# Optimization experiments

Measured on AMD Instinct MI355X. Metric: run time of the kernel, lower is better.

The kernel has to match this reference:

```python
import jax, jax.numpy as jnp
import numpy as np

N = 8192
IN_F = 512
OUT_F = 128
NUM_CLASSES = 10
ALPHA = 0.2  # LeakyReLU negative slope
NEG_INF = -9e15


def setup_inputs() -> dict:
    key = jax.random.key(0)
    k_h, k_d, k_W, k_a, k_cw, k_cb = jax.random.split(key, 6)
    h = jax.random.normal(k_h, (N, IN_F), dtype=jnp.float32)
    dist = jax.random.randint(k_d, (N, N), 0, 2, dtype=jnp.int32)
    # xavier_uniform with gain=1.414
    gain = 1.414
    lim_W = gain * np.sqrt(6.0 / (IN_F + OUT_F))
    W = jax.random.uniform(k_W, (IN_F, OUT_F), minval=-lim_W, maxval=lim_W, dtype=jnp.float32)
    lim_a = gain * np.sqrt(6.0 / (2 * OUT_F + 1))
    a = jax.random.uniform(k_a, (2 * OUT_F, 1), minval=-lim_a, maxval=lim_a, dtype=jnp.float32)
    # nn.Linear(out_features, num_classes): weight [C, out], bias [C]
    lim_c = np.sqrt(1.0 / OUT_F)
    Wc = jax.random.uniform(k_cw, (NUM_CLASSES, OUT_F), minval=-lim_c, maxval=lim_c, dtype=jnp.float32)
    bc = jax.random.uniform(k_cb, (NUM_CLASSES,), minval=-lim_c, maxval=lim_c, dtype=jnp.float32)
    return {"h": h, "dist": dist, "W": W, "a": a, "Wc": Wc, "bc": bc}


def reference(h, dist, W, a, Wc, bc):
    Wh = h @ W                              # [N, out]
    Wh1 = Wh @ a[:OUT_F]                    # [N, 1]
    Wh2 = Wh @ a[OUT_F:]                    # [N, 1]
    e = jax.nn.leaky_relu(Wh1 + Wh2.T, negative_slope=ALPHA)  # [N, N]
    att = jnp.where(dist > 0, e, NEG_INF)
    att = jax.nn.softmax(att, axis=1)       # [N, N]
    h_update = jax.nn.elu(att @ Wh)         # [N, out] (dropout inactive at inference)
    y_pred = h_update @ Wc.T + bc           # [N, num_classes]
    return y_pred
```

## Files before the change

### kernel.cpp

```cpp
#include <hip/hip_runtime.h>
#include <stdint.h>

#define N 8192
#define IN_F 512
#define OUT_F 128
#define NCLS 10
#define ALPHA 0.2f

typedef float f32x4 __attribute__((ext_vector_type(4)));
typedef int   i32x4 __attribute__((ext_vector_type(4)));
typedef short s16x4 __attribute__((ext_vector_type(4)));
typedef short s16x8 __attribute__((ext_vector_type(8)));

__device__ __forceinline__ short f2bf(float x) {
    unsigned u = __builtin_bit_cast(unsigned, x);
    u = (u + 0x7FFFu + ((u >> 16) & 1u)) >> 16;
    return (short)u;
}
__device__ __forceinline__ float bf2f(short s) {
    unsigned u = ((unsigned)(unsigned short)s) << 16;
    return __builtin_bit_cast(float, u);
}

__global__ __launch_bounds__(256, 8)
void mask_kernel(const int* __restrict__ dist, unsigned* __restrict__ mask) {
    size_t w = (size_t)blockIdx.x * 256 + threadIdx.x;
    const int* p = dist + w * 32;
    unsigned b = 0;
    #pragma unroll
    for (int u = 0; u < 8; ++u) {
        i32x4 v = *(const i32x4*)(p + u * 4);
        #pragma unroll
        for (int e = 0; e < 4; ++e) b |= (v[e] > 0 ? 1u : 0u) << (u * 4 + e);
    }
    mask[w] = b;
}

__global__ void split_w_kernel(const float* __restrict__ W,
                               short* __restrict__ WThi, short* __restrict__ WTlo) {
    int idx = blockIdx.x * 256 + threadIdx.x;
    int k = idx >> 7, col = idx & 127;
    float x = W[idx];
    short hi = f2bf(x);
    short lo = f2bf(x - bf2f(hi));
    size_t a = (size_t)(k >> 5) * (128 * 32) + (size_t)col * 32 + (k & 31);
    WThi[a] = hi;
    WTlo[a] = lo;
}

#define WH_ROWS 16
#define WH_STR 520

__global__ __launch_bounds__(256, 2)
void wh_kernel(const float* __restrict__ h, const short* __restrict__ WThi,
               const short* __restrict__ WTlo, const float* __restrict__ a,
               short* __restrict__ WhT, float* __restrict__ Wh1,
               float* __restrict__ Wh2) {
    __shared__ __align__(16) short Ahi[WH_ROWS][WH_STR];
    __shared__ __align__(16) short Alo[WH_ROWS][WH_STR];
    __shared__ __align__(16) float whs[WH_ROWS][OUT_F + 4];

    const int t = threadIdx.x;
    const int r0 = blockIdx.x * WH_ROWS;

    {
        int row = t >> 4, c4 = t & 15;
        const float* hrow = h + (size_t)(r0 + row) * IN_F;
        #pragma unroll
        for (int jj = 0; jj < 4; ++jj) {
            int k0 = c4 * 8 + jj * 128;
            f32x4 x0 = *(const f32x4*)(hrow + k0);
            f32x4 x1 = *(const f32x4*)(hrow + k0 + 4);
            s16x8 hi, lo;
            #pragma unroll
            for (int e = 0; e < 4; ++e) {
                short h0 = f2bf(x0[e]); hi[e] = h0; lo[e] = f2bf(x0[e] - bf2f(h0));
                short h1 = f2bf(x1[e]); hi[4 + e] = h1; lo[4 + e] = f2bf(x1[e] - bf2f(h1));
            }
            *(s16x8*)&Ahi[row][k0] = hi;
            *(s16x8*)&Alo[row][k0] = lo;
        }
    }
    __syncthreads();

    const int lane = t & 63, w = t >> 6;
    const int q = lane >> 4, ln16 = lane & 15;
    f32x4 acc[2] = {};
    #pragma unroll
    for (int kc = 0; kc < IN_F / 32; ++kc) {
        s16x8 ahi = *(const s16x8*)&Ahi[ln16][kc * 32 + q * 8];
        s16x8 alo = *(const s16x8*)&Alo[ln16][kc * 32 + q * 8];
        #pragma unroll
        for (int nt = 0; nt < 2; ++nt) {
            int col = w * 32 + nt * 16 + ln16;
            size_t boff = (size_t)kc * 4096 + (size_t)col * 32 + q * 8;
            s16x8 bhi = *(const s16x8*)(WThi + boff);
            s16x8 blo = *(const s16x8*)(WTlo + boff);
            acc[nt] = __builtin_amdgcn_mfma_f32_16x16x32_bf16(ahi, bhi, acc[nt], 0, 0, 0);
            acc[nt] = __builtin_amdgcn_mfma_f32_16x16x32_bf16(ahi, blo, acc[nt], 0, 0, 0);
            acc[nt] = __builtin_amdgcn_mfma_f32_16x16x32_bf16(alo, bhi, acc[nt], 0, 0, 0);
        }
    }
    #pragma unroll
    for (int nt = 0; nt < 2; ++nt)
        #pragma unroll
        for (int reg = 0; reg < 4; ++reg)
            whs[q * 4 + reg][w * 32 + nt * 16 + ln16] = acc[nt][reg];
    __syncthreads();

    if (t < 128) {
        int r = t >> 3, s = t & 7;
        float s1 = 0.f, s2 = 0.f;
        #pragma unroll
        for (int cc = 0; cc < 16; ++cc) {
            int c = s * 16 + cc;
            float v = whs[r][c];
            s1 = fmaf(v, a[c], s1);
            s2 = fmaf(v, a[OUT_F + c], s2);
        }
        s1 += __shfl_xor(s1, 1); s1 += __shfl_xor(s1, 2); s1 += __shfl_xor(s1, 4);
        s2 += __shfl_xor(s2, 1); s2 += __shfl_xor(s2, 2); s2 += __shfl_xor(s2, 4);
        if (s == 0) { Wh1[r0 + r] = s1; Wh2[r0 + r] = s2; }
    }

    {
        int c = t >> 1, h8 = t & 1;
        s16x8 pack;
        #pragma unroll
        for (int rr = 0; rr < 8; ++rr) pack[rr] = f2bf(whs[h8 * 8 + rr][c]);
        size_t addr = (size_t)(r0 >> 5) * 4096 + (size_t)c * 32 + (r0 & 16) + h8 * 8;
        *(s16x8*)(WhT + addr) = pack;
    }
}

#define BM 32
#define BK 256
#define ASTR (BK + 8)

__global__ __launch_bounds__(256, 4)
void attn_kernel(const unsigned* __restrict__ mask, const short* __restrict__ WhT,
                 const float* __restrict__ Wh1v, const float* __restrict__ Wh2v,
                 float* __restrict__ acc_part, float* __restrict__ l_part,
                 int nit) {
    __shared__ __align__(16) short As[2][BM][ASTR];

    const int t = threadIdx.x;
    const int it = blockIdx.x & 255;
    const int sp = blockIdx.x >> 8;
    const int i0 = it * BM;
    const int r = t >> 3, s = t & 7;
    const int lane = t & 63, w = t >> 6;
    const int q = lane >> 4, ln16 = lane & 15;
    const int j0 = sp * nit * BK;
    const int sh = s * 4;

    const unsigned* __restrict__ mrow = mask + (size_t)(i0 + r) * (N / 32) + (j0 >> 5);
    const float* __restrict__ wh2p = Wh2v + j0;
    const float wh1 = Wh1v[i0 + r];
    float l_acc = 0.f;
    f32x4 acc[2][2] = {};

    i32x4 m0 = *(const i32x4*)(mrow);
    i32x4 m1 = *(const i32x4*)(mrow + 4);

    for (int kt = 0; kt < nit; ++kt) {
        const int jb = kt * BK;
        const bool more = (kt + 1) < nit;
        i32x4 n0, n1;
        if (more) {
            n0 = *(const i32x4*)(mrow + (kt + 1) * 8);
            n1 = *(const i32x4*)(mrow + (kt + 1) * 8 + 4);
        }
        short* arow = &As[kt & 1][r][0];
        #pragma unroll
        for (int u = 0; u < 8; ++u) {
            f32x4 w2 = *(const f32x4*)(wh2p + jb + u * 32 + sh);
            unsigned wrd = (u < 4) ? (unsigned)m0[u] : (unsigned)m1[u - 4];
            unsigned nib = (wrd >> sh) & 15u;
            s16x4 pk;
            #pragma unroll
            for (int e = 0; e < 4; ++e) {
                float sv = wh1 + w2[e];
                float lr = fmaxf(sv, ALPHA * sv);
                float pv = (nib & (1u << e)) ? __expf(lr) : 0.f;
                l_acc += pv;
                pk[e] = f2bf(pv);
            }
            *(s16x4*)(arow + u * 32 + sh) = pk;
        }
        __syncthreads();
        const short* ab = &As[kt & 1][0][0];
        const short* bbase = WhT + (size_t)(j0 + jb) * 128;
        #pragma unroll
        for (int kc = 0; kc < BK / 32; ++kc) {
            s16x8 a0 = *(const s16x8*)(ab + ln16 * ASTR + kc * 32 + q * 8);
            s16x8 a1 = *(const s16x8*)(ab + (16 + ln16) * ASTR + kc * 32 + q * 8);
            #pragma unroll
            for (int nt = 0; nt < 2; ++nt) {
                int col = w * 32 + nt * 16 + ln16;
                s16x8 b = *(const s16x8*)(bbase + (size_t)kc * 4096 + col * 32 + q * 8);
                acc[0][nt] = __builtin_amdgcn_mfma_f32_16x16x32_bf16(a0, b, acc[0][nt], 0, 0, 0);
                acc[1][nt] = __builtin_amdgcn_mfma_f32_16x16x32_bf16(a1, b, acc[1][nt], 0, 0, 0);
            }
        }
        if (more) { m0 = n0; m1 = n1; }
    }

    l_acc += __shfl_xor(l_acc, 1);
    l_acc += __shfl_xor(l_acc, 2);
    l_acc += __shfl_xor(l_acc, 4);
    if (s == 0) l_part[(size_t)sp * N + i0 + r] = l_acc;

    float* ap = acc_part + (size_t)sp * N * OUT_F + (size_t)i0 * OUT_F;
    #pragma unroll
    for (int mt = 0; mt < 2; ++mt)
        #pragma unroll
        for (int reg = 0; reg < 4; ++reg) {
            int row = mt * 16 + q * 4 + reg;
            #pragma unroll
            for (int nt = 0; nt < 2; ++nt)
                ap[(size_t)row * OUT_F + w * 32 + nt * 16 + ln16] = acc[mt][nt][reg];
        }
}

__global__ __launch_bounds__(256, 4)
void reduce_kernel(const float* __restrict__ acc_part, const float* __restrict__ l_part,
                   const float* __restrict__ Wc, const float* __restrict__ bcv,
                   float* __restrict__ out, int split) {
    __shared__ __align__(16) float hu[16][OUT_F + 4];
    const int t = threadIdx.x;
    const int i0 = blockIdx.x * 16;
    const int row = t >> 4, cg = t & 15;

    f32x4 v0 = {0.f, 0.f, 0.f, 0.f}, v1 = {0.f, 0.f, 0.f, 0.f};
    float l = 0.f;
    for (int s = 0; s < split; ++s) {
        const float* ap = acc_part + (size_t)s * N * OUT_F + (size_t)(i0 + row) * OUT_F + cg * 8;
        v0 += *(const f32x4*)ap;
        v1 += *(const f32x4*)(ap + 4);
        l += l_part[(size_t)s * N + i0 + row];
    }
    float inv = 1.f / l;
    #pragma unroll
    for (int e = 0; e < 4; ++e) {
        float x0 = v0[e] * inv; x0 = x0 > 0.f ? x0 : (__expf(x0) - 1.f);
        float x1 = v1[e] * inv; x1 = x1 > 0.f ? x1 : (__expf(x1) - 1.f);
        hu[row][cg * 8 + e] = x0;
        hu[row][cg * 8 + 4 + e] = x1;
    }
    __syncthreads();

    if (t < 16 * NCLS) {
        int rr = t / NCLS, cls = t - rr * NCLS;
        const f32x4* hurow = (const f32x4*)&hu[rr][0];
        const f32x4* wcrow = (const f32x4*)(Wc + cls * OUT_F);
        float sum = bcv[cls];
        #pragma unroll 8
        for (int c4 = 0; c4 < OUT_F / 4; ++c4) {
            f32x4 hv = hurow[c4];
            f32x4 wv = wcrow[c4];
            sum += hv[0] * wv[0] + hv[1] * wv[1] + hv[2] * wv[2] + hv[3] * wv[3];
        }
        out[(size_t)(i0 + rr) * NCLS + cls] = sum;
    }
}

extern "C" void kernel_launch(void* const* d_in, const int* in_sizes, int n_in,
                              void* d_out, int out_size, void* d_ws, size_t ws_size,
                              hipStream_t stream) {
    const float* h    = (const float*)d_in[0];
    const int*   dist = (const int*)d_in[1];
    const float* W    = (const float*)d_in[2];
    const float* a    = (const float*)d_in[3];
    const float* Wc   = (const float*)d_in[4];
    const float* bc   = (const float*)d_in[5];
    float* out = (float*)d_out;

    char* ws = (char*)d_ws;
    size_t off = 0;
    short* WhT  = (short*)(ws + off); off += (size_t)OUT_F * N * 2;
    short* WThi = (short*)(ws + off); off += (size_t)IN_F * OUT_F * 2;
    short* WTlo = (short*)(ws + off); off += (size_t)IN_F * OUT_F * 2;
    float* Wh1  = (float*)(ws + off); off += (size_t)N * 4;
    float* Wh2  = (float*)(ws + off); off += (size_t)N * 4;
    unsigned* mask = (unsigned*)(ws + off); off += (size_t)N * (N / 32) * 4;

    size_t per_split = (size_t)N * OUT_F * 4 + (size_t)N * 4;
    int split = 4;
    if (off + 4 * per_split > ws_size) split = 2;
    if (off + 2 * per_split > ws_size) split = 1;
    float* acc_part = (float*)(ws + off); off += (size_t)split * N * OUT_F * 4;
    float* l_part   = (float*)(ws + off);

    hipLaunchKernelGGL(mask_kernel, dim3(N * (N / 32) / 256), dim3(256), 0, stream,
                       dist, mask);
    hipLaunchKernelGGL(split_w_kernel, dim3(256), dim3(256), 0, stream, W, WThi, WTlo);
    hipLaunchKernelGGL(wh_kernel, dim3(N / WH_ROWS), dim3(256), 0, stream,
                       h, WThi, WTlo, a, WhT, Wh1, Wh2);
    int nit = N / (BK * split);
    hipLaunchKernelGGL(attn_kernel, dim3(256 * split), dim3(256), 0, stream,
                       mask, WhT, Wh1, Wh2, acc_part, l_part, nit);
    hipLaunchKernelGGL(reduce_kernel, dim3(N / 16), dim3(256), 0, stream,
                       acc_part, l_part, Wc, bc, out, split);
}
```

Before: 437.1 us.

## Halve attention K tile, stage Wh2 slice in LDS, fix split at compile time

Cuts the attention kernel's K tile from 256 to 128 columns and raises launch bounds to 6 waves/SIMD to allow more occupancy. Each block now preloads its whole 2048-element Wh2 slice into shared memory once, instead of reading it from global memory every tile. The split count becomes a compile-time constant of 4 and the workspace-size fallback is removed. That adds 8 KB of LDS per block and doubles the number of loop iterations and barriers.

```diff
diff --git a/kernel.cpp b/kernel.cpp
--- a/kernel.cpp
+++ b/kernel.cpp
@@ -134,15 +134,18 @@
 }
 
 #define BM 32
-#define BK 256
+#define BK 128
 #define ASTR (BK + 8)
-
-__global__ __launch_bounds__(256, 4)
+#define SPLIT 4
+#define NIT (N / (BK * SPLIT))
+#define JSPAN (N / SPLIT)
+
+__global__ __launch_bounds__(256, 6)
 void attn_kernel(const unsigned* __restrict__ mask, const short* __restrict__ WhT,
                  const float* __restrict__ Wh1v, const float* __restrict__ Wh2v,
-                 float* __restrict__ acc_part, float* __restrict__ l_part,
-                 int nit) {
+                 float* __restrict__ acc_part, float* __restrict__ l_part) {
     __shared__ __align__(16) short As[2][BM][ASTR];
+    __shared__ __align__(16) float wh2s[JSPAN];
 
     const int t = threadIdx.x;
     const int it = blockIdx.x & 255;
@@ -151,32 +154,33 @@
     const int r = t >> 3, s = t & 7;
     const int lane = t & 63, w = t >> 6;
     const int q = lane >> 4, ln16 = lane & 15;
-    const int j0 = sp * nit * BK;
+    const int j0 = sp * JSPAN;
     const int sh = s * 4;
 
+    {
+        f32x4 a0 = *(const f32x4*)(Wh2v + j0 + t * 8);
+        f32x4 a1 = *(const f32x4*)(Wh2v + j0 + t * 8 + 4);
+        *(f32x4*)&wh2s[t * 8] = a0;
+        *(f32x4*)&wh2s[t * 8 + 4] = a1;
+    }
+
     const unsigned* __restrict__ mrow = mask + (size_t)(i0 + r) * (N / 32) + (j0 >> 5);
-    const float* __restrict__ wh2p = Wh2v + j0;
     const float wh1 = Wh1v[i0 + r];
     float l_acc = 0.f;
     f32x4 acc[2][2] = {};
 
-    i32x4 m0 = *(const i32x4*)(mrow);
-    i32x4 m1 = *(const i32x4*)(mrow + 4);
-
-    for (int kt = 0; kt < nit; ++kt) {
+    i32x4 m = *(const i32x4*)mrow;
+    __syncthreads();
+
+    for (int kt = 0; kt < NIT; ++kt) {
         const int jb = kt * BK;
-        const bool more = (kt + 1) < nit;
-        i32x4 n0, n1;
-        if (more) {
-            n0 = *(const i32x4*)(mrow + (kt + 1) * 8);
-            n1 = *(const i32x4*)(mrow + (kt + 1) * 8 + 4);
-        }
+        i32x4 mn = m;
+        if (kt + 1 < NIT) mn = *(const i32x4*)(mrow + (kt + 1) * 4);
         short* arow = &As[kt & 1][r][0];
         #pragma unroll
-        for (int u = 0; u < 8; ++u) {
-            f32x4 w2 = *(const f32x4*)(wh2p + jb + u * 32 + sh);
-            unsigned wrd = (u < 4) ? (unsigned)m0[u] : (unsigned)m1[u - 4];
-            unsigned nib = (wrd >> sh) & 15u;
+        for (int u = 0; u < 4; ++u) {
+            f32x4 w2 = *(const f32x4*)&wh2s[jb + u * 32 + sh];
+            unsigned nib = ((unsigned)m[u] >> sh) & 15u;
             s16x4 pk;
             #pragma unroll
             for (int e = 0; e < 4; ++e) {
@@ -203,7 +207,7 @@
                 acc[1][nt] = __builtin_amdgcn_mfma_f32_16x16x32_bf16(a1, b, acc[1][nt], 0, 0, 0);
             }
         }
-        if (more) { m0 = n0; m1 = n1; }
+        m = mn;
     }
 
     l_acc += __shfl_xor(l_acc, 1);
@@ -285,11 +289,7 @@
     float* Wh2  = (float*)(ws + off); off += (size_t)N * 4;
     unsigned* mask = (unsigned*)(ws + off); off += (size_t)N * (N / 32) * 4;
 
-    size_t per_split = (size_t)N * OUT_F * 4 + (size_t)N * 4;
-    int split = 4;
-    if (off + 4 * per_split > ws_size) split = 2;
-    if (off + 2 * per_split > ws_size) split = 1;
-    float* acc_part = (float*)(ws + off); off += (size_t)split * N * OUT_F * 4;
+    float* acc_part = (float*)(ws + off); off += (size_t)SPLIT * N * OUT_F * 4;
     float* l_part   = (float*)(ws + off);
 
     hipLaunchKernelGGL(mask_kernel, dim3(N * (N / 32) / 256), dim3(256), 0, stream,
@@ -297,9 +297,8 @@
     hipLaunchKernelGGL(split_w_kernel, dim3(256), dim3(256), 0, stream, W, WThi, WTlo);
     hipLaunchKernelGGL(wh_kernel, dim3(N / WH_ROWS), dim3(256), 0, stream,
                        h, WThi, WTlo, a, WhT, Wh1, Wh2);
-    int nit = N / (BK * split);
-    hipLaunchKernelGGL(attn_kernel, dim3(256 * split), dim3(256), 0, stream,
-                       mask, WhT, Wh1, Wh2, acc_part, l_part, nit);
+    hipLaunchKernelGGL(attn_kernel, dim3(256 * SPLIT), dim3(256), 0, stream,
+                       mask, WhT, Wh1, Wh2, acc_part, l_part);
     hipLaunchKernelGGL(reduce_kernel, dim3(N / 16), dim3(256), 0, stream,
-                       acc_part, l_part, Wc, bc, out, split);
-}
+                       acc_part, l_part, Wc, bc, out, SPLIT);
+}
```

Measured after the change: 443.4 us. No clear change (+1.5%).

## Streamline attention probability path: exp2 prescale, packed bf16 cvt, MFMA row sums

Applied to the files above, without the earlier changes.

Pre-scales Wh1/Wh2 by log2(e) so the attention kernel can call the hardware exp2 directly, which is valid because LeakyReLU is positively homogeneous. It replaces manual bf16 rounding with the packed v_cvt_pk_bf16_f32 instruction. The softmax denominator is now computed by an MFMA against a ones vector on two waves, replacing per-thread adds and shuffles; this also makes l consistent with the bf16-rounded probabilities. The split count and iteration count become compile-time constants, dropping the workspace-size fallback.

```diff
diff --git a/kernel.cpp b/kernel.cpp
--- a/kernel.cpp
+++ b/kernel.cpp
@@ -6,11 +6,13 @@
 #define OUT_F 128
 #define NCLS 10
 #define ALPHA 0.2f
+#define LOG2E 1.44269504088896340736f
 
 typedef float f32x4 __attribute__((ext_vector_type(4)));
 typedef int   i32x4 __attribute__((ext_vector_type(4)));
 typedef short s16x4 __attribute__((ext_vector_type(4)));
 typedef short s16x8 __attribute__((ext_vector_type(8)));
+typedef unsigned u32x2 __attribute__((ext_vector_type(2)));
 
 __device__ __forceinline__ short f2bf(float x) {
     unsigned u = __builtin_bit_cast(unsigned, x);
@@ -120,7 +122,7 @@
         }
         s1 += __shfl_xor(s1, 1); s1 += __shfl_xor(s1, 2); s1 += __shfl_xor(s1, 4);
         s2 += __shfl_xor(s2, 1); s2 += __shfl_xor(s2, 2); s2 += __shfl_xor(s2, 4);
-        if (s == 0) { Wh1[r0 + r] = s1; Wh2[r0 + r] = s2; }
+        if (s == 0) { Wh1[r0 + r] = s1 * LOG2E; Wh2[r0 + r] = s2 * LOG2E; }
     }
 
     {
@@ -136,12 +138,17 @@
 #define BM 32
 #define BK 256
 #define ASTR (BK + 8)
+#define SPLIT 4
+#define NIT (N / (BK * SPLIT))
+
+__device__ __forceinline__ f32x4 mfma16(s16x8 a, s16x8 b, f32x4 c) {
+    return __builtin_amdgcn_mfma_f32_16x16x32_bf16(a, b, c, 0, 0, 0);
+}
 
 __global__ __launch_bounds__(256, 4)
 void attn_kernel(const unsigned* __restrict__ mask, const short* __restrict__ WhT,
                  const float* __restrict__ Wh1v, const float* __restrict__ Wh2v,
-                 float* __restrict__ acc_part, float* __restrict__ l_part,
-                 int nit) {
+                 float* __restrict__ acc_part, float* __restrict__ l_part) {
     __shared__ __align__(16) short As[2][BM][ASTR];
 
     const int t = threadIdx.x;
@@ -151,21 +158,25 @@
     const int r = t >> 3, s = t & 7;
     const int lane = t & 63, w = t >> 6;
     const int q = lane >> 4, ln16 = lane & 15;
-    const int j0 = sp * nit * BK;
+    const int j0 = sp * (NIT * BK);
     const int sh = s * 4;
 
     const unsigned* __restrict__ mrow = mask + (size_t)(i0 + r) * (N / 32) + (j0 >> 5);
     const float* __restrict__ wh2p = Wh2v + j0;
     const float wh1 = Wh1v[i0 + r];
-    float l_acc = 0.f;
     f32x4 acc[2][2] = {};
+    f32x4 accl = {};
+
+    s16x8 bones;
+    #pragma unroll
+    for (int e = 0; e < 8; ++e) bones[e] = (short)0x3F80;
 
     i32x4 m0 = *(const i32x4*)(mrow);
     i32x4 m1 = *(const i32x4*)(mrow + 4);
 
-    for (int kt = 0; kt < nit; ++kt) {
+    for (int kt = 0; kt < NIT; ++kt) {
         const int jb = kt * BK;
-        const bool more = (kt + 1) < nit;
+        const bool more = (kt + 1) < NIT;
         i32x4 n0, n1;
         if (more) {
             n0 = *(const i32x4*)(mrow + (kt + 1) * 8);
@@ -177,16 +188,19 @@
             f32x4 w2 = *(const f32x4*)(wh2p + jb + u * 32 + sh);
             unsigned wrd = (u < 4) ? (unsigned)m0[u] : (unsigned)m1[u - 4];
             unsigned nib = (wrd >> sh) & 15u;
-            s16x4 pk;
+            float p[4];
             #pragma unroll
             for (int e = 0; e < 4; ++e) {
                 float sv = wh1 + w2[e];
                 float lr = fmaxf(sv, ALPHA * sv);
-                float pv = (nib & (1u << e)) ? __expf(lr) : 0.f;
-                l_acc += pv;
-                pk[e] = f2bf(pv);
+                float ev = __builtin_amdgcn_exp2f(lr);
+                p[e] = (nib & (1u << e)) ? ev : 0.f;
             }
-            *(s16x4*)(arow + u * 32 + sh) = pk;
+            unsigned pk01, pk23;
+            asm("v_cvt_pk_bf16_f32 %0, %1, %2" : "=v"(pk01) : "v"(p[0]), "v"(p[1]));
+            asm("v_cvt_pk_bf16_f32 %0, %1, %2" : "=v"(pk23) : "v"(p[2]), "v"(p[3]));
+            u32x2 pk = {pk01, pk23};
+            *(u32x2*)(arow + u * 32 + sh) = pk;
         }
         __syncthreads();
         const short* ab = &As[kt & 1][0][0];
@@ -195,21 +209,24 @@
         for (int kc = 0; kc < BK / 32; ++kc) {
             s16x8 a0 = *(const s16x8*)(ab + ln16 * ASTR + kc * 32 + q * 8);
             s16x8 a1 = *(const s16x8*)(ab + (16 + ln16) * ASTR + kc * 32 + q * 8);
+            if (w == 0) accl = mfma16(a0, bones, accl);
+            if (w == 1) accl = mfma16(a1, bones, accl);
             #pragma unroll
             for (int nt = 0; nt < 2; ++nt) {
                 int col = w * 32 + nt * 16 + ln16;
                 s16x8 b = *(const s16x8*)(bbase + (size_t)kc * 4096 + col * 32 + q * 8);
-                acc[0][nt] = __builtin_amdgcn_mfma_f32_16x16x32_bf16(a0, b, acc[0][nt], 0, 0, 0);
-                acc[1][nt] = __builtin_amdgcn_mfma_f32_16x16x32_bf16(a1, b, acc[1][nt], 0, 0, 0);
+                acc[0][nt] = mfma16(a0, b, acc[0][nt]);
+                acc[1][nt] = mfma16(a1, b, acc[1][nt]);
             }
         }
         if (more) { m0 = n0; m1 = n1; }
     }
 
-    l_acc += __shfl_xor(l_acc, 1);
-    l_acc += __shfl_xor(l_acc, 2);
-    l_acc += __shfl_xor(l_acc, 4);
-    if (s == 0) l_part[(size_t)sp * N + i0 + r] = l_acc;
+    if (w < 2 && ln16 == 0) {
+        #pragma unroll
+        for (int reg = 0; reg < 4; ++reg)
+            l_part[(size_t)sp * N + i0 + w * 16 + q * 4 + reg] = accl[reg];
+    }
 
     float* ap = acc_part + (size_t)sp * N * OUT_F + (size_t)i0 * OUT_F;
     #pragma unroll
@@ -285,11 +302,7 @@
     float* Wh2  = (float*)(ws + off); off += (size_t)N * 4;
     unsigned* mask = (unsigned*)(ws + off); off += (size_t)N * (N / 32) * 4;
 
-    size_t per_split = (size_t)N * OUT_F * 4 + (size_t)N * 4;
-    int split = 4;
-    if (off + 4 * per_split > ws_size) split = 2;
-    if (off + 2 * per_split > ws_size) split = 1;
-    float* acc_part = (float*)(ws + off); off += (size_t)split * N * OUT_F * 4;
+    float* acc_part = (float*)(ws + off); off += (size_t)SPLIT * N * OUT_F * 4;
     float* l_part   = (float*)(ws + off);
 
     hipLaunchKernelGGL(mask_kernel, dim3(N * (N / 32) / 256), dim3(256), 0, stream,
@@ -297,9 +310,8 @@
     hipLaunchKernelGGL(split_w_kernel, dim3(256), dim3(256), 0, stream, W, WThi, WTlo);
     hipLaunchKernelGGL(wh_kernel, dim3(N / WH_ROWS), dim3(256), 0, stream,
                        h, WThi, WTlo, a, WhT, Wh1, Wh2);
-    int nit = N / (BK * split);
-    hipLaunchKernelGGL(attn_kernel, dim3(256 * split), dim3(256), 0, stream,
-                       mask, WhT, Wh1, Wh2, acc_part, l_part, nit);
+    hipLaunchKernelGGL(attn_kernel, dim3(256 * SPLIT), dim3(256), 0, stream,
+                       mask, WhT, Wh1, Wh2, acc_part, l_part);
     hipLaunchKernelGGL(reduce_kernel, dim3(N / 16), dim3(256), 0, stream,
-                       acc_part, l_part, Wc, bc, out, split);
-}
+                       acc_part, l_part, Wc, bc, out, SPLIT);
+}
```

After: 438.2 us. About the same (+0.3%).
